# Kernel tuning notes

Hardware: AMD Instinct MI355X
Metric: run time of the kernel (lower is better)

The kernel has to match this reference:

```python
import jax, jax.numpy as jnp
import numpy as np

B, T, F = 512, 1024, 128
H, LH, OUT = 512, 1024, 1

def setup_inputs() -> dict:
    key = jax.random.key(0)
    ks = jax.random.split(key, 9)
    s_ih = 1.0 / np.sqrt(H)
    return {
        "x":    jax.random.normal(ks[0], (B, T, F), dtype=jnp.float32),
        # torch nn.LSTM params: weight_ih_l0 [4H,F], weight_hh_l0 [4H,H], biases [4H]
        "W_ih": jax.random.uniform(ks[1], (4 * H, F), minval=-s_ih, maxval=s_ih, dtype=jnp.float32),
        "W_hh": jax.random.uniform(ks[2], (4 * H, H), minval=-s_ih, maxval=s_ih, dtype=jnp.float32),
        "b_ih": jax.random.uniform(ks[3], (4 * H,), minval=-s_ih, maxval=s_ih, dtype=jnp.float32),
        "b_hh": jax.random.uniform(ks[4], (4 * H,), minval=-s_ih, maxval=s_ih, dtype=jnp.float32),
        # head: Linear(H, LH) -> ReLU -> Linear(LH, OUT)
        "W1": jax.random.normal(ks[5], (LH, H), dtype=jnp.float32) * (1.0 / np.sqrt(H)),
        "b1": jnp.zeros((LH,), dtype=jnp.float32),
        "W2": jax.random.normal(ks[6], (OUT, LH), dtype=jnp.float32) * (1.0 / np.sqrt(LH)),
        "b2": jnp.zeros((OUT,), dtype=jnp.float32),
    }

def _lstm_last_h(x, W_ih, W_hh, b_ih, b_hh):
    # x: [B,T,F]; returns final hidden state h_T: [B,H]
    b = x.shape[0]
    h0 = jnp.zeros((b, W_hh.shape[1]), dtype=x.dtype)
    c0 = h0
    xs = jnp.swapaxes(x, 0, 1)  # [T,B,F]
    # precompute input projections for all timesteps in one big GEMM
    x_proj = jnp.einsum('tbf,gf->tbg', xs, W_ih) + b_ih + b_hh  # [T,B,4H]
    hidden = W_hh.shape[1]

    def step(carry, xp):
        h, c = carry
        gates = xp + h @ W_hh.T  # [B,4H]
        i, f, g, o = jnp.split(gates, 4, axis=-1)
        i = jax.nn.sigmoid(i)
        f = jax.nn.sigmoid(f)
        g = jnp.tanh(g)
        o = jax.nn.sigmoid(o)
        c = f * c + i * g
        h = o * jnp.tanh(c)
        return (h, c), None

    (hT, _), _ = jax.lax.scan(step, (h0, c0), x_proj)
    return hT

def reference(x, W_ih, W_hh, b_ih, b_hh, W1, b1, W2, b2):
    hT = _lstm_last_h(x, W_ih, W_hh, b_ih, b_hh)        # [B,H]
    z = jax.nn.relu(hT @ W1.T + b1)                     # [B,LH] (dropout: eval/identity)
    out = z @ W2.T + b2                                 # [B,OUT]
    return out[..., None]                               # [B,OUT,1]
```

## Files before the change

kernel.cpp:

```cpp
#include <hip/hip_runtime.h>

typedef unsigned short u16;
typedef unsigned int u32;
typedef __attribute__((ext_vector_type(8))) short bf16x8;
typedef __attribute__((ext_vector_type(4))) float f32x4;
typedef __attribute__((ext_vector_type(4))) unsigned int u32x4;

#define B_ 512
#define T_ 1024
#define F_ 128
#define H_ 512
#define G_ 2048
#define LH_ 1024

#define MFMA16(a,b,c) (c) = __builtin_amdgcn_mfma_f32_16x16x32_bf16((a),(b),(c),0,0,0)

__device__ __forceinline__ u16 f2bf(float f) {
  unsigned u = __float_as_uint(f);
  unsigned r = (u + 0x7fffu + ((u >> 16) & 1u)) >> 16;
  return (u16)r;
}
__device__ __forceinline__ float bf2f(u16 h) {
  return __uint_as_float(((unsigned)h) << 16);
}

constexpr size_t O_HPK     = 0;
constexpr size_t O_FL      = O_HPK + (size_t)2 * B_ * H_ * 2;
constexpr size_t O_MSET    = O_FL + 4096;
constexpr size_t O_WHH_HI  = O_MSET;
constexpr size_t O_WHH_LO  = O_WHH_HI + (size_t)G_ * H_ * 2;
constexpr size_t O_WIH_HI  = O_WHH_LO + (size_t)G_ * H_ * 2;
constexpr size_t O_WIH_LO  = O_WIH_HI + (size_t)G_ * F_ * 2;
constexpr size_t O_BIAS    = O_WIH_LO + (size_t)G_ * F_ * 2;
constexpr size_t O_HT      = O_BIAS + (size_t)G_ * 4;
constexpr size_t O_Z       = O_HT + (size_t)B_ * H_ * 4;

constexpr unsigned SM_WHH_LO = 65536;
constexpr unsigned SM_XC     = 131072;
constexpr unsigned SM_BIAS   = 147456;
constexpr unsigned SMEM_BYTES = 147712;

__global__ void prep_weights(const float* __restrict__ Wih, const float* __restrict__ Whh,
                             const float* __restrict__ bih, const float* __restrict__ bhh,
                             u16* __restrict__ WhhHi, u16* __restrict__ WhhLo,
                             u16* __restrict__ WihHi, u16* __restrict__ WihLo,
                             float* __restrict__ bias) {
  int P = blockIdx.x;
  int nb = P >> 6, g = (P >> 4) & 3, u = P & 15;
  int orig = g * H_ + (nb << 4) + u;
  for (int k = threadIdx.x; k < H_; k += 128) {
    float w = Whh[(size_t)orig * H_ + k];
    u16 hi = f2bf(w);
    WhhHi[(size_t)P * H_ + k] = hi;
    WhhLo[(size_t)P * H_ + k] = f2bf(w - bf2f(hi));
  }
  {
    int k = threadIdx.x;
    float w = Wih[(size_t)orig * F_ + k];
    u16 hi = f2bf(w);
    WihHi[(size_t)P * F_ + k] = hi;
    WihLo[(size_t)P * F_ + k] = f2bf(w - bf2f(hi));
  }
  if (threadIdx.x == 0) bias[P] = bih[orig] + bhh[orig];
}

__device__ __forceinline__ u32x4 ald16(const u16* p) {
  u32x4 r;
  asm volatile("global_load_dwordx4 %0, %1, off sc1" : "=&v"(r) : "v"(p));
  return r;
}
__device__ __forceinline__ u32x4 pld16(const float* p) {
  u32x4 r;
  asm volatile("global_load_dwordx4 %0, %1, off" : "=&v"(r) : "v"(p));
  return r;
}
__device__ __forceinline__ void ast2(u16* p, u16 v) {
  asm volatile("global_store_short %0, %1, off sc1" :: "v"(p), "v"((u32)v) : "memory");
}

__device__ __forceinline__ void cvt8(u32x4 a, u32x4 b, bf16x8& hi, bf16x8& lo) {
  #pragma unroll
  for (int j = 0; j < 8; ++j) {
    float f = __uint_as_float(j < 4 ? a[j] : b[j - 4]);
    u16 h = f2bf(f);
    hi[j] = (short)h;
    lo[j] = (short)f2bf(f - bf2f(h));
  }
}

__device__ __forceinline__ bf16x8 ldB(const u16* base, int r, int k8) {
  return *(const bf16x8*)(base + r * 512 + ((k8 ^ (r & 63)) << 3));
}

__global__ __launch_bounds__(512, 2) void lstm_persistent(
    const float* __restrict__ x,
    const u16* __restrict__ WhhHi, const u16* __restrict__ WhhLo,
    const u16* __restrict__ WihHi, const u16* __restrict__ WihLo,
    const float* __restrict__ bias,
    u16* __restrict__ hPk, u32* __restrict__ fl, float* __restrict__ hT) {
  extern __shared__ char smem[];
  u16* sWhhHi  = (u16*)(smem);
  u16* sWhhLo  = (u16*)(smem + SM_WHH_LO);
  float* sXc   = (float*)(smem + SM_XC);
  float* sBias = (float*)(smem + SM_BIAS);

  const int tid = threadIdx.x;
  const int w = tid >> 6, l = tid & 63;
  const int m  = blockIdx.x & 7;
  const int nb = blockIdx.x >> 3;
  const int Pbase = 64 * nb;
  const int l15 = l & 15, l4 = l >> 4;
  const int rt = w >> 1, cp = w & 1;

  for (int i = tid; i < 4096; i += 512) {
    int r = i >> 6, k8 = i & 63;
    unsigned dst = r * 512 + ((k8 ^ (r & 63)) << 3);
    *(bf16x8*)(sWhhHi + dst) = *(const bf16x8*)(WhhHi + (size_t)(Pbase + r) * H_ + k8 * 8);
    *(bf16x8*)(sWhhLo + dst) = *(const bf16x8*)(WhhLo + (size_t)(Pbase + r) * H_ + k8 * 8);
  }
  if (tid < 64) sBias[tid] = bias[Pbase + tid];

  bf16x8 wfh[4][2], wfl[4][2];
  #pragma unroll
  for (int ct = 0; ct < 4; ++ct)
    #pragma unroll
    for (int ch = 0; ch < 2; ++ch) {
      int gcol = 16 * ct + l15;
      int k8i = 8 * cp + 4 * ch + l4;
      wfh[ct][ch] = *(const bf16x8*)(WihHi + (size_t)(Pbase + gcol) * F_ + k8i * 8);
      wfl[ct][ch] = *(const bf16x8*)(WihLo + (size_t)(Pbase + gcol) * F_ + k8i * 8);
    }
  __syncthreads();

  const float bi = sBias[l15], bf_ = sBias[16 + l15], bg = sBias[32 + l15], bo = sBias[48 + l15];
  const int arow = 64 * m + 16 * rt + l15;

  u32x4 xa[2], xb[2];
  {
    const float* xr = x + (size_t)arow * T_ * F_ + 64 * cp + 8 * l4;
    xa[0] = pld16(xr);      xb[0] = pld16(xr + 4);
    xa[1] = pld16(xr + 32); xb[1] = pld16(xr + 36);
  }
  asm volatile("s_waitcnt vmcnt(0)" ::: "memory");

  float cr[4] = {0.f, 0.f, 0.f, 0.f};

  #pragma unroll 1
  for (int t = 0; t < T_; ++t) {
    const u16* hcur = hPk + (size_t)(t & 1) * B_ * H_;
    u16* hnxt = hPk + (size_t)((t & 1) ^ 1) * B_ * H_;

    f32x4 acc0 = {0.f,0.f,0.f,0.f}, acc1 = {0.f,0.f,0.f,0.f};
    f32x4 acc2 = {0.f,0.f,0.f,0.f}, acc3 = {0.f,0.f,0.f,0.f};

    if (t > 0 && l < 16) {
      const u32* fp = fl + m * 32 + 16 * cp + l;
      long fuse = 400000000;
      while (__hip_atomic_load(fp, __ATOMIC_RELAXED, __HIP_MEMORY_SCOPE_AGENT) < (u32)t) {
        __builtin_amdgcn_s_sleep(1);
        if (--fuse == 0) break;
      }
    }

    u32x4 Aa[8];
    const u16* hrowt = hcur + (size_t)arow * H_ + 256 * cp + 8 * l4;
    if (t > 0) {
      #pragma unroll
      for (int c = 0; c < 8; ++c) Aa[c] = ald16(hrowt + c * 32);
    }

    #pragma unroll
    for (int ch = 0; ch < 2; ++ch) {
      bf16x8 xh, xl;
      cvt8(xa[ch], xb[ch], xh, xl);
      MFMA16(xh, wfh[0][ch], acc0); MFMA16(xl, wfh[0][ch], acc0); MFMA16(xh, wfl[0][ch], acc0);
      MFMA16(xh, wfh[1][ch], acc1); MFMA16(xl, wfh[1][ch], acc1); MFMA16(xh, wfl[1][ch], acc1);
      MFMA16(xh, wfh[2][ch], acc2); MFMA16(xl, wfh[2][ch], acc2); MFMA16(xh, wfl[2][ch], acc2);
      MFMA16(xh, wfh[3][ch], acc3); MFMA16(xl, wfh[3][ch], acc3); MFMA16(xh, wfl[3][ch], acc3);
    }

    if (t > 0) {
      #pragma unroll
      for (int ch = 0; ch < 8; ++ch) {
        if (ch == 0)      asm volatile("s_waitcnt vmcnt(7)");
        else if (ch == 1) asm volatile("s_waitcnt vmcnt(6)");
        else if (ch == 2) asm volatile("s_waitcnt vmcnt(5)");
        else if (ch == 3) asm volatile("s_waitcnt vmcnt(4)");
        else if (ch == 4) asm volatile("s_waitcnt vmcnt(3)");
        else if (ch == 5) asm volatile("s_waitcnt vmcnt(2)");
        else if (ch == 6) asm volatile("s_waitcnt vmcnt(1)");
        else              asm volatile("s_waitcnt vmcnt(0)");
        __builtin_amdgcn_sched_barrier(0);
        bf16x8 ah = *(const bf16x8*)&Aa[ch];
        int k8 = 32 * cp + 4 * ch + l4;
        bf16x8 bh, bl;
        bh = ldB(sWhhHi, l15, k8);      bl = ldB(sWhhLo, l15, k8);
        MFMA16(ah, bh, acc0); MFMA16(ah, bl, acc0);
        bh = ldB(sWhhHi, 16 + l15, k8); bl = ldB(sWhhLo, 16 + l15, k8);
        MFMA16(ah, bh, acc1); MFMA16(ah, bl, acc1);
        bh = ldB(sWhhHi, 32 + l15, k8); bl = ldB(sWhhLo, 32 + l15, k8);
        MFMA16(ah, bh, acc2); MFMA16(ah, bl, acc2);
        bh = ldB(sWhhHi, 48 + l15, k8); bl = ldB(sWhhLo, 48 + l15, k8);
        MFMA16(ah, bh, acc3); MFMA16(ah, bl, acc3);
      }
    }

    if (cp == 1) {
      float* bse = sXc + (rt * 16) * 64 + l;
      bse[0 * 64]  = acc0[0]; bse[1 * 64]  = acc0[1]; bse[2 * 64]  = acc0[2]; bse[3 * 64]  = acc0[3];
      bse[4 * 64]  = acc1[0]; bse[5 * 64]  = acc1[1]; bse[6 * 64]  = acc1[2]; bse[7 * 64]  = acc1[3];
      bse[8 * 64]  = acc2[0]; bse[9 * 64]  = acc2[1]; bse[10 * 64] = acc2[2]; bse[11 * 64] = acc2[3];
      bse[12 * 64] = acc3[0]; bse[13 * 64] = acc3[1]; bse[14 * 64] = acc3[2]; bse[15 * 64] = acc3[3];
    }

    __syncthreads();

    {
      int tp = (t + 1 < T_) ? t + 1 : 0;
      const float* xr = x + (size_t)arow * T_ * F_ + (size_t)tp * F_ + 64 * cp + 8 * l4;
      xa[0] = pld16(xr);      xb[0] = pld16(xr + 4);
      xa[1] = pld16(xr + 32); xb[1] = pld16(xr + 36);
    }

    if (cp == 0) {
      const float* bse = sXc + (rt * 16) * 64 + l;
      float p[16];
      #pragma unroll
      for (int j = 0; j < 16; ++j) p[j] = bse[j * 64];
      #pragma unroll
      for (int q = 0; q < 4; ++q) {
        float gi = acc0[q] + p[q]      + bi;
        float gf = acc1[q] + p[4 + q]  + bf_;
        float gg = acc2[q] + p[8 + q]  + bg;
        float go = acc3[q] + p[12 + q] + bo;
        float ii = 1.f / (1.f + __expf(-gi));
        float ff = 1.f / (1.f + __expf(-gf));
        float gG = 1.f - 2.f / (__expf(2.f * gg) + 1.f);
        float oo = 1.f / (1.f + __expf(-go));
        float c = ff * cr[q] + ii * gG;
        cr[q] = c;
        float h = oo * (1.f - 2.f / (__expf(2.f * c) + 1.f));
        size_t idx = (size_t)(64 * m + 16 * rt + 4 * l4 + q) * H_ + 16 * nb + l15;
        ast2(&hnxt[idx], f2bf(h));
        if (t == T_ - 1) hT[idx] = h;
      }
    }

    asm volatile("s_waitcnt vmcnt(0)" ::: "memory");
    __syncthreads();
    if (tid == 0) {
      __hip_atomic_store(&fl[m * 32 + nb], (u32)(t + 1), __ATOMIC_RELAXED, __HIP_MEMORY_SCOPE_AGENT);
      asm volatile("s_waitcnt vmcnt(0)" ::: "memory");
    }
  }
}

__global__ __launch_bounds__(256) void head1(const float* __restrict__ hT,
                                             const float* __restrict__ W1,
                                             const float* __restrict__ b1,
                                             float* __restrict__ z) {
  __shared__ float sA[64][16];
  __shared__ float sBt[16][64];
  int tx = threadIdx.x & 15, ty = threadIdx.x >> 4;
  int row0 = blockIdx.y * 64, col0 = blockIdx.x * 64;
  float acc[4][4] = {};
  for (int k0 = 0; k0 < H_; k0 += 16) {
    int c = threadIdx.x >> 2, kk4 = (threadIdx.x & 3) * 4;
    float4 av = *(const float4*)(hT + (size_t)(row0 + c) * H_ + k0 + kk4);
    *(float4*)&sA[c][kk4] = av;
    float4 bv = *(const float4*)(W1 + (size_t)(col0 + c) * H_ + k0 + kk4);
    sBt[kk4 + 0][c] = bv.x; sBt[kk4 + 1][c] = bv.y;
    sBt[kk4 + 2][c] = bv.z; sBt[kk4 + 3][c] = bv.w;
    __syncthreads();
    #pragma unroll
    for (int kk = 0; kk < 16; ++kk) {
      float a0 = sA[ty * 4 + 0][kk], a1 = sA[ty * 4 + 1][kk];
      float a2 = sA[ty * 4 + 2][kk], a3 = sA[ty * 4 + 3][kk];
      float b0 = sBt[kk][tx * 4 + 0], b1v = sBt[kk][tx * 4 + 1];
      float b2v = sBt[kk][tx * 4 + 2], b3 = sBt[kk][tx * 4 + 3];
      acc[0][0] += a0 * b0; acc[0][1] += a0 * b1v; acc[0][2] += a0 * b2v; acc[0][3] += a0 * b3;
      acc[1][0] += a1 * b0; acc[1][1] += a1 * b1v; acc[1][2] += a1 * b2v; acc[1][3] += a1 * b3;
      acc[2][0] += a2 * b0; acc[2][1] += a2 * b1v; acc[2][2] += a2 * b2v; acc[2][3] += a2 * b3;
      acc[3][0] += a3 * b0; acc[3][1] += a3 * b1v; acc[3][2] += a3 * b2v; acc[3][3] += a3 * b3;
    }
    __syncthreads();
  }
  #pragma unroll
  for (int i = 0; i < 4; ++i)
    #pragma unroll
    for (int j = 0; j < 4; ++j) {
      int rr = row0 + ty * 4 + i, cc = col0 + tx * 4 + j;
      float v = acc[i][j] + b1[cc];
      z[(size_t)rr * LH_ + cc] = v > 0.f ? v : 0.f;
    }
}

__global__ __launch_bounds__(256) void head2(const float* __restrict__ z,
                                             const float* __restrict__ W2,
                                             const float* __restrict__ b2,
                                             float* __restrict__ out) {
  int b = blockIdx.x;
  float p = 0.f;
  for (int j = threadIdx.x; j < LH_; j += 256) p += z[(size_t)b * LH_ + j] * W2[j];
  #pragma unroll
  for (int off = 32; off > 0; off >>= 1) p += __shfl_down(p, off);
  __shared__ float red[4];
  if ((threadIdx.x & 63) == 0) red[threadIdx.x >> 6] = p;
  __syncthreads();
  if (threadIdx.x == 0) out[b] = red[0] + red[1] + red[2] + red[3] + b2[0];
}

extern "C" void kernel_launch(void* const* d_in, const int* in_sizes, int n_in,
                              void* d_out, int out_size, void* d_ws, size_t ws_size,
                              hipStream_t stream) {
  const float* x    = (const float*)d_in[0];
  const float* Wih  = (const float*)d_in[1];
  const float* Whh  = (const float*)d_in[2];
  const float* bih  = (const float*)d_in[3];
  const float* bhh  = (const float*)d_in[4];
  const float* W1   = (const float*)d_in[5];
  const float* b1   = (const float*)d_in[6];
  const float* W2   = (const float*)d_in[7];
  const float* b2   = (const float*)d_in[8];

  char* ws = (char*)d_ws;
  u16* hPk      = (u16*)(ws + O_HPK);
  u32* fl       = (u32*)(ws + O_FL);
  u16* whhHi    = (u16*)(ws + O_WHH_HI);
  u16* whhLo    = (u16*)(ws + O_WHH_LO);
  u16* wihHi    = (u16*)(ws + O_WIH_HI);
  u16* wihLo    = (u16*)(ws + O_WIH_LO);
  float* bias   = (float*)(ws + O_BIAS);
  float* hT     = (float*)(ws + O_HT);
  float* zbuf   = (float*)(ws + O_Z);

  (void)hipMemsetAsync(ws, 0, O_MSET, stream);

  prep_weights<<<G_, 128, 0, stream>>>(Wih, Whh, bih, bhh, whhHi, whhLo, wihHi, wihLo, bias);

  (void)hipFuncSetAttribute((const void*)lstm_persistent,
                            hipFuncAttributeMaxDynamicSharedMemorySize, SMEM_BYTES);

  lstm_persistent<<<256, 512, SMEM_BYTES, stream>>>(x, whhHi, whhLo, wihHi, wihLo,
                                                    bias, hPk, fl, hT);

  head1<<<dim3(LH_ / 64, B_ / 64), 256, 0, stream>>>(hT, W1, b1, zbuf);
  head2<<<B_, 256, 0, stream>>>(zbuf, W2, b2, (float*)d_out);
}
```

Before: 6.927 ms.

## Split LSTM gate columns across twice as many persistent blocks with swapped MFMA operands

```diff
diff --git a/kernel.cpp b/kernel.cpp
--- a/kernel.cpp
+++ b/kernel.cpp
@@ -35,10 +35,9 @@
 constexpr size_t O_HT      = O_BIAS + (size_t)G_ * 4;
 constexpr size_t O_Z       = O_HT + (size_t)B_ * H_ * 4;
 
-constexpr unsigned SM_WHH_LO = 65536;
-constexpr unsigned SM_XC     = 131072;
-constexpr unsigned SM_BIAS   = 147456;
-constexpr unsigned SMEM_BYTES = 147712;
+constexpr unsigned SM_WHH_LO = 32768;
+constexpr unsigned SM_XC     = 65536;
+constexpr unsigned SMEM_BYTES = 73728;
 
 __global__ void prep_weights(const float* __restrict__ Wih, const float* __restrict__ Whh,
                              const float* __restrict__ bih, const float* __restrict__ bhh,
@@ -46,8 +45,8 @@
                              u16* __restrict__ WihHi, u16* __restrict__ WihLo,
                              float* __restrict__ bias) {
   int P = blockIdx.x;
-  int nb = P >> 6, g = (P >> 4) & 3, u = P & 15;
-  int orig = g * H_ + (nb << 4) + u;
+  int nb = P >> 5, s = P & 31, u2 = s >> 2, g = s & 3;
+  int orig = g * H_ + 8 * nb + u2;
   for (int k = threadIdx.x; k < H_; k += 128) {
     float w = Whh[(size_t)orig * H_ + k];
     u16 hi = f2bf(w);
@@ -89,10 +88,10 @@
 }
 
 __device__ __forceinline__ bf16x8 ldB(const u16* base, int r, int k8) {
-  return *(const bf16x8*)(base + r * 512 + ((k8 ^ (r & 63)) << 3));
-}
-
-__global__ __launch_bounds__(512, 2) void lstm_persistent(
+  return *(const bf16x8*)(base + r * 512 + ((k8 ^ r) << 3));
+}
+
+__global__ __launch_bounds__(512, 4) void lstm_persistent(
     const float* __restrict__ x,
     const u16* __restrict__ WhhHi, const u16* __restrict__ WhhLo,
     const u16* __restrict__ WihHi, const u16* __restrict__ WihLo,
@@ -102,37 +101,41 @@
   u16* sWhhHi  = (u16*)(smem);
   u16* sWhhLo  = (u16*)(smem + SM_WHH_LO);
   float* sXc   = (float*)(smem + SM_XC);
-  float* sBias = (float*)(smem + SM_BIAS);
 
   const int tid = threadIdx.x;
   const int w = tid >> 6, l = tid & 63;
   const int m  = blockIdx.x & 7;
   const int nb = blockIdx.x >> 3;
-  const int Pbase = 64 * nb;
+  const int Pbase = 32 * nb;
   const int l15 = l & 15, l4 = l >> 4;
   const int rt = w >> 1, cp = w & 1;
 
-  for (int i = tid; i < 4096; i += 512) {
+  for (int i = tid; i < 2048; i += 512) {
     int r = i >> 6, k8 = i & 63;
-    unsigned dst = r * 512 + ((k8 ^ (r & 63)) << 3);
+    unsigned dst = r * 512 + ((k8 ^ r) << 3);
     *(bf16x8*)(sWhhHi + dst) = *(const bf16x8*)(WhhHi + (size_t)(Pbase + r) * H_ + k8 * 8);
     *(bf16x8*)(sWhhLo + dst) = *(const bf16x8*)(WhhLo + (size_t)(Pbase + r) * H_ + k8 * 8);
   }
-  if (tid < 64) sBias[tid] = bias[Pbase + tid];
-
-  bf16x8 wfh[4][2], wfl[4][2];
-  #pragma unroll
-  for (int ct = 0; ct < 4; ++ct)
+
+  float bg[2][4];
+  #pragma unroll
+  for (int ct = 0; ct < 2; ++ct)
+    #pragma unroll
+    for (int q = 0; q < 4; ++q)
+      bg[ct][q] = bias[Pbase + 16 * ct + 4 * l4 + q];
+
+  bf16x8 wfh[2][2], wfl[2][2];
+  #pragma unroll
+  for (int ct = 0; ct < 2; ++ct)
     #pragma unroll
     for (int ch = 0; ch < 2; ++ch) {
-      int gcol = 16 * ct + l15;
+      int gr = 16 * ct + l15;
       int k8i = 8 * cp + 4 * ch + l4;
-      wfh[ct][ch] = *(const bf16x8*)(WihHi + (size_t)(Pbase + gcol) * F_ + k8i * 8);
-      wfl[ct][ch] = *(const bf16x8*)(WihLo + (size_t)(Pbase + gcol) * F_ + k8i * 8);
+      wfh[ct][ch] = *(const bf16x8*)(WihHi + (size_t)(Pbase + gr) * F_ + k8i * 8);
+      wfl[ct][ch] = *(const bf16x8*)(WihLo + (size_t)(Pbase + gr) * F_ + k8i * 8);
     }
   __syncthreads();
 
-  const float bi = sBias[l15], bf_ = sBias[16 + l15], bg = sBias[32 + l15], bo = sBias[48 + l15];
   const int arow = 64 * m + 16 * rt + l15;
 
   u32x4 xa[2], xb[2];
@@ -143,7 +146,7 @@
   }
   asm volatile("s_waitcnt vmcnt(0)" ::: "memory");
 
-  float cr[4] = {0.f, 0.f, 0.f, 0.f};
+  float cr[2] = {0.f, 0.f};
 
   #pragma unroll 1
   for (int t = 0; t < T_; ++t) {
@@ -151,10 +154,9 @@
     u16* hnxt = hPk + (size_t)((t & 1) ^ 1) * B_ * H_;
 
     f32x4 acc0 = {0.f,0.f,0.f,0.f}, acc1 = {0.f,0.f,0.f,0.f};
-    f32x4 acc2 = {0.f,0.f,0.f,0.f}, acc3 = {0.f,0.f,0.f,0.f};
-
-    if (t > 0 && l < 16) {
-      const u32* fp = fl + m * 32 + 16 * cp + l;
+
+    if (t > 0 && l < 32) {
+      const u32* fp = fl + m * 64 + 32 * cp + l;
       long fuse = 400000000;
       while (__hip_atomic_load(fp, __ATOMIC_RELAXED, __HIP_MEMORY_SCOPE_AGENT) < (u32)t) {
         __builtin_amdgcn_s_sleep(1);
@@ -173,10 +175,8 @@
     for (int ch = 0; ch < 2; ++ch) {
       bf16x8 xh, xl;
       cvt8(xa[ch], xb[ch], xh, xl);
-      MFMA16(xh, wfh[0][ch], acc0); MFMA16(xl, wfh[0][ch], acc0); MFMA16(xh, wfl[0][ch], acc0);
-      MFMA16(xh, wfh[1][ch], acc1); MFMA16(xl, wfh[1][ch], acc1); MFMA16(xh, wfl[1][ch], acc1);
-      MFMA16(xh, wfh[2][ch], acc2); MFMA16(xl, wfh[2][ch], acc2); MFMA16(xh, wfl[2][ch], acc2);
-      MFMA16(xh, wfh[3][ch], acc3); MFMA16(xl, wfh[3][ch], acc3); MFMA16(xh, wfl[3][ch], acc3);
+      MFMA16(wfh[0][ch], xh, acc0); MFMA16(wfh[0][ch], xl, acc0); MFMA16(wfl[0][ch], xh, acc0);
+      MFMA16(wfh[1][ch], xh, acc1); MFMA16(wfh[1][ch], xl, acc1); MFMA16(wfl[1][ch], xh, acc1);
     }
 
     if (t > 0) {
@@ -191,26 +191,20 @@
         else if (ch == 6) asm volatile("s_waitcnt vmcnt(1)");
         else              asm volatile("s_waitcnt vmcnt(0)");
         __builtin_amdgcn_sched_barrier(0);
-        bf16x8 ah = *(const bf16x8*)&Aa[ch];
+        bf16x8 hb = *(const bf16x8*)&Aa[ch];
         int k8 = 32 * cp + 4 * ch + l4;
         bf16x8 bh, bl;
         bh = ldB(sWhhHi, l15, k8);      bl = ldB(sWhhLo, l15, k8);
-        MFMA16(ah, bh, acc0); MFMA16(ah, bl, acc0);
+        MFMA16(bh, hb, acc0); MFMA16(bl, hb, acc0);
         bh = ldB(sWhhHi, 16 + l15, k8); bl = ldB(sWhhLo, 16 + l15, k8);
-        MFMA16(ah, bh, acc1); MFMA16(ah, bl, acc1);
-        bh = ldB(sWhhHi, 32 + l15, k8); bl = ldB(sWhhLo, 32 + l15, k8);
-        MFMA16(ah, bh, acc2); MFMA16(ah, bl, acc2);
-        bh = ldB(sWhhHi, 48 + l15, k8); bl = ldB(sWhhLo, 48 + l15, k8);
-        MFMA16(ah, bh, acc3); MFMA16(ah, bl, acc3);
+        MFMA16(bh, hb, acc1); MFMA16(bl, hb, acc1);
       }
     }
 
     if (cp == 1) {
-      float* bse = sXc + (rt * 16) * 64 + l;
-      bse[0 * 64]  = acc0[0]; bse[1 * 64]  = acc0[1]; bse[2 * 64]  = acc0[2]; bse[3 * 64]  = acc0[3];
-      bse[4 * 64]  = acc1[0]; bse[5 * 64]  = acc1[1]; bse[6 * 64]  = acc1[2]; bse[7 * 64]  = acc1[3];
-      bse[8 * 64]  = acc2[0]; bse[9 * 64]  = acc2[1]; bse[10 * 64] = acc2[2]; bse[11 * 64] = acc2[3];
-      bse[12 * 64] = acc3[0]; bse[13 * 64] = acc3[1]; bse[14 * 64] = acc3[2]; bse[15 * 64] = acc3[3];
+      float* bse = sXc + rt * 512 + l;
+      bse[0 * 64] = acc0[0]; bse[1 * 64] = acc0[1]; bse[2 * 64] = acc0[2]; bse[3 * 64] = acc0[3];
+      bse[4 * 64] = acc1[0]; bse[5 * 64] = acc1[1]; bse[6 * 64] = acc1[2]; bse[7 * 64] = acc1[3];
     }
 
     __syncthreads();
@@ -223,24 +217,25 @@
     }
 
     if (cp == 0) {
-      const float* bse = sXc + (rt * 16) * 64 + l;
-      float p[16];
+      const float* bse = sXc + rt * 512 + l;
+      float p[8];
       #pragma unroll
-      for (int j = 0; j < 16; ++j) p[j] = bse[j * 64];
+      for (int j = 0; j < 8; ++j) p[j] = bse[j * 64];
       #pragma unroll
-      for (int q = 0; q < 4; ++q) {
-        float gi = acc0[q] + p[q]      + bi;
-        float gf = acc1[q] + p[4 + q]  + bf_;
-        float gg = acc2[q] + p[8 + q]  + bg;
-        float go = acc3[q] + p[12 + q] + bo;
+      for (int ct = 0; ct < 2; ++ct) {
+        const f32x4& a = ct ? acc1 : acc0;
+        float gi = a[0] + p[ct * 4 + 0] + bg[ct][0];
+        float gf = a[1] + p[ct * 4 + 1] + bg[ct][1];
+        float gg = a[2] + p[ct * 4 + 2] + bg[ct][2];
+        float go = a[3] + p[ct * 4 + 3] + bg[ct][3];
         float ii = 1.f / (1.f + __expf(-gi));
         float ff = 1.f / (1.f + __expf(-gf));
         float gG = 1.f - 2.f / (__expf(2.f * gg) + 1.f);
         float oo = 1.f / (1.f + __expf(-go));
-        float c = ff * cr[q] + ii * gG;
-        cr[q] = c;
+        float c = ff * cr[ct] + ii * gG;
+        cr[ct] = c;
         float h = oo * (1.f - 2.f / (__expf(2.f * c) + 1.f));
-        size_t idx = (size_t)(64 * m + 16 * rt + 4 * l4 + q) * H_ + 16 * nb + l15;
+        size_t idx = (size_t)arow * H_ + 8 * nb + 4 * ct + l4;
         ast2(&hnxt[idx], f2bf(h));
         if (t == T_ - 1) hT[idx] = h;
       }
@@ -249,7 +244,7 @@
     asm volatile("s_waitcnt vmcnt(0)" ::: "memory");
     __syncthreads();
     if (tid == 0) {
-      __hip_atomic_store(&fl[m * 32 + nb], (u32)(t + 1), __ATOMIC_RELAXED, __HIP_MEMORY_SCOPE_AGENT);
+      __hip_atomic_store(&fl[m * 64 + nb], (u32)(t + 1), __ATOMIC_RELAXED, __HIP_MEMORY_SCOPE_AGENT);
       asm volatile("s_waitcnt vmcnt(0)" ::: "memory");
     }
   }
@@ -341,7 +336,7 @@
   (void)hipFuncSetAttribute((const void*)lstm_persistent,
                             hipFuncAttributeMaxDynamicSharedMemorySize, SMEM_BYTES);
 
-  lstm_persistent<<<256, 512, SMEM_BYTES, stream>>>(x, whhHi, whhLo, wihHi, wihLo,
+  lstm_persistent<<<512, 512, SMEM_BYTES, stream>>>(x, whhHi, whhLo, wihHi, wihLo,
                                                     bias, hPk, fl, hT);
 
   head1<<<dim3(LH_ / 64, B_ / 64), 256, 0, stream>>>(hT, W1, b1, zbuf);
```

Measured after the change: 16.41 ms. 2.37x slower.
